# Optimization experiments

Measured on AMD Instinct MI355X. Metric: run time of the kernel, lower is better.

## Reference

```python
import jax, jax.numpy as jnp
import numpy as np

N = 50000        # num nodes
E = 800000       # num edges (before self loops)
F_DIM = 256      # embedding_dim
H = 4            # num_heads
C = 64           # latent_dim
SLOPE = 0.2      # PyG GATConv leaky_relu negative_slope


def setup_inputs() -> dict:
    key = jax.random.key(0)
    ks = jax.random.split(key, 11)
    s = 0.05
    return {
        "x": jax.random.normal(ks[0], (N, F_DIM), jnp.float32),
        "edge_index": jax.random.randint(ks[1], (2, E), 0, N),
        "W1": jax.random.normal(ks[2], (F_DIM, H * C), jnp.float32) * s,
        "a_src1": jax.random.normal(ks[3], (H, C), jnp.float32) * s,
        "a_dst1": jax.random.normal(ks[4], (H, C), jnp.float32) * s,
        "b1": jnp.zeros((H * C,), jnp.float32),
        "W2": jax.random.normal(ks[5], (H * C, F_DIM), jnp.float32) * s,
        "a_src2": jax.random.normal(ks[6], (1, F_DIM), jnp.float32) * s,
        "a_dst2": jax.random.normal(ks[7], (1, F_DIM), jnp.float32) * s,
        "b2": jnp.zeros((F_DIM,), jnp.float32),
    }


def gat_layer(x, src, dst, W, a_src, a_dst, bias, heads, out_ch):
    n = x.shape[0]
    xW = (x @ W).reshape(n, heads, out_ch)              # [N,H,C]
    alpha_s = jnp.sum(xW * a_src, axis=-1)               # [N,H]
    alpha_d = jnp.sum(xW * a_dst, axis=-1)               # [N,H]
    e = jax.nn.leaky_relu(alpha_s[src] + alpha_d[dst], SLOPE)  # [E,H]
    m = jax.ops.segment_max(e, dst, num_segments=n)      # segment-softmax over in-edges
    w = jnp.exp(e - m[dst])
    z = jax.ops.segment_sum(w, dst, num_segments=n)
    alpha = w / z[dst]                                    # [E,H]
    out = jax.ops.segment_sum(xW[src] * alpha[:, :, None], dst, num_segments=n)  # [N,H,C]
    return out.reshape(n, heads * out_ch) + bias          # concat=True


def reference(x, edge_index, W1, a_src1, a_dst1, b1, W2, a_src2, a_dst2, b2):
    loop = jnp.arange(N)  # PyG default add_self_loops=True
    src = jnp.concatenate([edge_index[0], loop])
    dst = jnp.concatenate([edge_index[1], loop])
    h = jax.nn.elu(gat_layer(x, src, dst, W1, a_src1, a_dst1, b1, H, C))
    return gat_layer(h, src, dst, W2, a_src2, a_dst2, b2, 1, F_DIM)
```

## Files before the change

### kernel.cpp

```cpp
#include <hip/hip_runtime.h>
#include <hip/hip_bf16.h>
#include <math.h>

#define N_NODES 50000
#define N_EDGES 800000
#define ETOT    (N_EDGES + N_NODES)
#define FDIM    256
#define SLOPE   0.2f

typedef __bf16    bf16x8 __attribute__((ext_vector_type(8)));
typedef float     f32x4  __attribute__((ext_vector_type(4)));
typedef _Float16  f16x8  __attribute__((ext_vector_type(8)));
typedef _Float16  f16x4  __attribute__((ext_vector_type(4)));

__global__ void count_edges(const int* __restrict__ dst, int* __restrict__ counts) {
    int i = blockIdx.x * blockDim.x + threadIdx.x;
    if (i < N_EDGES) atomicAdd(&counts[dst[i]], 1);
}

__global__ void scan1(const int* __restrict__ counts, int* __restrict__ partial,
                      int* __restrict__ blockSums) {
    __shared__ int wsum[4];
    int b = blockIdx.x, t = threadIdx.x;
    int base = b * 1024;
    int i0 = base + t * 4;
    int v[4];
#pragma unroll
    for (int u = 0; u < 4; u++) { int i = i0 + u; v[u] = (i < N_NODES) ? (counts[i] + 1) : 0; }
    v[1] += v[0]; v[2] += v[1]; v[3] += v[2];
    int lane = t & 63, wid = t >> 6;
    int incl = v[3];
#pragma unroll
    for (int d = 1; d < 64; d <<= 1) {
        int o = __shfl_up(incl, d, 64);
        if (lane >= d) incl += o;
    }
    if (lane == 63) wsum[wid] = incl;
    __syncthreads();
    int woff = 0;
#pragma unroll
    for (int w = 0; w < 4; w++) if (w < wid) woff += wsum[w];
    int texcl = woff + incl - v[3];
#pragma unroll
    for (int u = 0; u < 4; u++) { int i = i0 + u; if (i < N_NODES) partial[i] = texcl + v[u]; }
    if (t == 255) blockSums[b] = woff + incl;
}

__global__ void scan3(const int* __restrict__ partial, const int* __restrict__ blockSums,
                      int* __restrict__ row_ptr, int* __restrict__ cursor) {
    int b = blockIdx.x, t = threadIdx.x;
    __shared__ int s_off;
    if (t < 64) {
        int v = (t < b) ? blockSums[t] : 0;
#pragma unroll
        for (int d = 1; d < 64; d <<= 1) v += __shfl_xor(v, d, 64);
        if (t == 0) s_off = v;
    }
    __syncthreads();
    int off = s_off;
    int base = b * 1024;
#pragma unroll
    for (int u = 0; u < 4; u++) {
        int i = base + t + u * 256;
        if (i < N_NODES) {
            row_ptr[i + 1] = off + partial[i];
            cursor[i]      = off + ((i == base) ? 0 : partial[i - 1]);
        }
    }
    if (b == 0 && t == 0) row_ptr[0] = 0;
}

__global__ void scatter_edges(const int* __restrict__ src, const int* __restrict__ dst,
                              int* __restrict__ cursor, int* __restrict__ col_src) {
    int i = blockIdx.x * blockDim.x + threadIdx.x;
    if (i >= ETOT) return;
    int s, d;
    if (i < N_EDGES) { s = src[i]; d = dst[i]; }
    else             { s = i - N_EDGES; d = s; }
    int p = atomicAdd(&cursor[d], 1);
    col_src[p] = s;
}

__global__ void pack_w2(const float* __restrict__ W1, const float* __restrict__ W2,
                        __bf16* __restrict__ P1, __bf16* __restrict__ P2) {
    int tid = blockIdx.x * 256 + threadIdx.x;
    const float* W = (tid < 65536) ? W1 : W2;
    __bf16* P = (tid < 65536) ? P1 : P2;
    int t = tid & 65535;
    int j    = t & 7;
    int lane = (t >> 3) & 63;
    int nb   = (t >> 9) & 3;
    int w    = (t >> 11) & 3;
    int step = (t >> 13) & 7;
    int col = (w << 6) | (nb << 4) | (lane & 15);
    int k   = (step << 5) | ((lane >> 4) << 3) | j;
    float v = W[(k << 8) | col];
    __bf16 h = (__bf16)v;
    int base = (((((step << 2) | w) << 2) | nb) << 10) | (lane << 3) | j;
    P[base]       = h;
    P[base + 512] = (__bf16)(v - (float)h);
}

template <int HEADS, typename AT>
__global__ __launch_bounds__(256) void gemm_mfma(
        const AT* __restrict__ A, const __bf16* __restrict__ Bpk,
        _Float16* __restrict__ Ch,
        const float* __restrict__ avS, const float* __restrict__ avD,
        float* __restrict__ aS, float* __restrict__ aD, int M) {
    constexpr int LDA = 40;
    constexpr int LDC = 272;
    __shared__ union SMem {
        struct { __bf16 Ah[2][128 * LDA]; __bf16 Al[2][128 * LDA]; } st;
        _Float16 cts[64][LDC];
    } smem;
    __shared__ float sred[2][64][4];

    const int t = threadIdx.x;
    const int w = t >> 6, l = t & 63;
    const int q = l >> 4, c16 = l & 15;
    const int row0 = blockIdx.x * 128;

    const int ar = t >> 1, ak = (t & 1) << 4;
    const bool arow_ok = (row0 + ar) < M;
    const AT* Arow = A + (size_t)(row0 + ar) * 256 + ak;

    f32x4 acc[8][4];
#pragma unroll
    for (int i = 0; i < 8; i++)
#pragma unroll
        for (int j = 0; j < 4; j++) acc[i][j] = (f32x4){0.f, 0.f, 0.f, 0.f};

    float4 pv[4];
    f16x8  pvh[2];
#pragma unroll
    for (int i = 0; i < 4; i++) pv[i] = make_float4(0.f, 0.f, 0.f, 0.f);
    pvh[0] = (f16x8){0,0,0,0,0,0,0,0}; pvh[1] = pvh[0];
    if (arow_ok) {
        if constexpr (sizeof(AT) == 4) {
#pragma unroll
            for (int i = 0; i < 4; i++) pv[i] = *(const float4*)(Arow + (i << 2));
        } else {
            pvh[0] = *(const f16x8*)(Arow);
            pvh[1] = *(const f16x8*)(Arow + 8);
        }
    }

    for (int step = 0; step < 8; ++step) {
        const int k0 = step << 5;
        const int buf = step & 1;

        {
            float vv[16];
            if constexpr (sizeof(AT) == 4) {
#pragma unroll
                for (int i = 0; i < 4; i++) {
                    vv[i * 4 + 0] = pv[i].x; vv[i * 4 + 1] = pv[i].y;
                    vv[i * 4 + 2] = pv[i].z; vv[i * 4 + 3] = pv[i].w;
                }
            } else {
#pragma unroll
                for (int i = 0; i < 16; i++) vv[i] = (float)pvh[i >> 3][i & 7];
            }
            bf16x8 hv[2], lv[2];
#pragma unroll
            for (int i = 0; i < 16; i++) {
                __bf16 hb = (__bf16)vv[i];
                hv[i >> 3][i & 7] = hb;
                lv[i >> 3][i & 7] = (__bf16)(vv[i] - (float)hb);
            }
            *(bf16x8*)(&smem.st.Ah[buf][ar * LDA + ak])     = hv[0];
            *(bf16x8*)(&smem.st.Ah[buf][ar * LDA + ak + 8]) = hv[1];
            *(bf16x8*)(&smem.st.Al[buf][ar * LDA + ak])     = lv[0];
            *(bf16x8*)(&smem.st.Al[buf][ar * LDA + ak + 8]) = lv[1];
        }
        if (step < 7 && arow_ok) {
            if constexpr (sizeof(AT) == 4) {
#pragma unroll
                for (int i = 0; i < 4; i++) pv[i] = *(const float4*)(Arow + k0 + 32 + (i << 2));
            } else {
                pvh[0] = *(const f16x8*)(Arow + k0 + 32);
                pvh[1] = *(const f16x8*)(Arow + k0 + 40);
            }
        }
        const __bf16* Bs = Bpk + ((size_t)((step << 2) | w) << 12);
        bf16x8 bh[4], bl[4];
#pragma unroll
        for (int nb = 0; nb < 4; nb++) {
            bh[nb] = *(const bf16x8*)(Bs + (nb << 10) + (l << 3));
            bl[nb] = *(const bf16x8*)(Bs + (nb << 10) + 512 + (l << 3));
        }
        __syncthreads();

#pragma unroll
        for (int mb = 0; mb < 8; mb++) {
            int off = (c16 + (mb << 4)) * LDA + (q << 3);
            bf16x8 ah  = *(const bf16x8*)(&smem.st.Ah[buf][off]);
            bf16x8 alo = *(const bf16x8*)(&smem.st.Al[buf][off]);
#pragma unroll
            for (int nb = 0; nb < 4; nb++) {
                acc[mb][nb] = __builtin_amdgcn_mfma_f32_16x16x32_bf16(ah,  bh[nb], acc[mb][nb], 0, 0, 0);
                acc[mb][nb] = __builtin_amdgcn_mfma_f32_16x16x32_bf16(ah,  bl[nb], acc[mb][nb], 0, 0, 0);
                acc[mb][nb] = __builtin_amdgcn_mfma_f32_16x16x32_bf16(alo, bh[nb], acc[mb][nb], 0, 0, 0);
            }
        }
    }

#pragma unroll
    for (int half = 0; half < 2; ++half) {
        __syncthreads();
#pragma unroll
        for (int mbl = 0; mbl < 4; mbl++) {
            const int mb = (half << 2) | mbl;
#pragma unroll
            for (int r = 0; r < 4; r++) {
                int row = (mbl << 4) + (q << 2) + r;
                float s = 0.f, d = 0.f;
#pragma unroll
                for (int nb = 0; nb < 4; nb++) {
                    int col = (w << 6) + (nb << 4) + c16;
                    float val = acc[mb][nb][r];
                    s = fmaf(val, avS[col], s);
                    d = fmaf(val, avD[col], d);
                    smem.cts[row][col] = (_Float16)val;
                }
#pragma unroll
                for (int dd = 1; dd < 16; dd <<= 1) {
                    s += __shfl_xor(s, dd, 64);
                    d += __shfl_xor(d, dd, 64);
                }
                if (c16 == 0) { sred[0][row][w] = s; sred[1][row][w] = d; }
            }
        }
        __syncthreads();

        {
            const int crow = t >> 2;
            const int grow = row0 + (half << 6) + crow;
            if (grow < M) {
                _Float16* dstp = Ch + (size_t)grow * 256;
#pragma unroll
                for (int i = 0; i < 8; i++) {
                    int col = ((t & 3) << 3) + (i << 5);
                    *(f16x8*)(dstp + col) = *(const f16x8*)(&smem.cts[crow][col]);
                }
            }
        }
        if (HEADS == 4) {
            int row = t >> 2, wv = t & 3;
            int v = row0 + (half << 6) + row;
            if (v < M) { aS[v * 4 + wv] = sred[0][row][wv]; aD[v * 4 + wv] = sred[1][row][wv]; }
        } else {
            if (t < 64) {
                int v = row0 + (half << 6) + t;
                if (v < M) {
                    aS[v] = sred[0][t][0] + sred[0][t][1] + sred[0][t][2] + sred[0][t][3];
                    aD[v] = sred[1][t][0] + sred[1][t][1] + sred[1][t][2] + sred[1][t][3];
                }
            }
        }
    }
}

template <int HEADS, bool ELU, typename OT>
__global__ __launch_bounds__(256) void gat_aggregate_wave(
        const _Float16* __restrict__ xWh, const float* __restrict__ aS,
        const float* __restrict__ aD, const int* __restrict__ row_ptr,
        const int* __restrict__ col_src, const float* __restrict__ bias,
        OT* __restrict__ out) {
    const int wid  = threadIdx.x >> 6;
    const int lane = threadIdx.x & 63;
    const int v = blockIdx.x * 4 + wid;
    if (v >= N_NODES) return;

    constexpr int CH = 64 / HEADS;
    const int h = (HEADS == 4) ? (lane >> 4) : 0;
    const int q = (HEADS == 4) ? (lane & 15) : lane;

    const int half = lane >> 5;
    const int fl   = lane & 31;
    const int hf   = (HEADS == 4) ? (fl >> 3) : 0;
    const int wbase = (HEADS == 4) ? (hf << 4) : 0;

    const int beg = row_ptr[v], end = row_ptr[v + 1];
    const float adv = aD[v * HEADS + h];

    float acc[8] = {0.f, 0.f, 0.f, 0.f, 0.f, 0.f, 0.f, 0.f};
    float z = 0.f;
    for (int j0 = beg; j0 < end; j0 += CH) {
        const int cnt = min(CH, end - j0);
        int s = 0;
        float wgt = 0.f;
        if (q < cnt) {
            s = col_src[j0 + q];
            float e = aS[s * HEADS + h] + adv;
            e = (e > 0.f) ? e : SLOPE * e;
            wgt = __expf(e);
        }
        z += wgt;
        for (int jj = 0; jj < cnt; jj += 2) {
            const int qm = jj + half;
            const int sl = wbase | qm;
            const int   sj = __shfl(s,   sl, 64);
            const float wj = __shfl(wgt, sl, 64);
            if (qm < cnt) {
                const f16x8 row = *(const f16x8*)(xWh + ((size_t)sj << 8) + (fl << 3));
#pragma unroll
                for (int i = 0; i < 8; i++)
                    acc[i] = fmaf(wj, (float)row[i], acc[i]);
            }
        }
    }
#pragma unroll
    for (int d = 1; d < CH; d <<= 1) z += __shfl_xor(z, d, 64);
    const float zf = (HEADS == 4) ? __shfl(z, hf << 4, 64) : z;

#pragma unroll
    for (int i = 0; i < 8; i++) acc[i] += __shfl_xor(acc[i], 32, 64);

    const float rz = 1.f / zf;
    const int fbase = (fl << 3) + (half << 2);
    const float4 bv = *(const float4*)(bias + fbase);
    float4 o;
    o.x = acc[(half << 2) + 0] * rz + bv.x;
    o.y = acc[(half << 2) + 1] * rz + bv.y;
    o.z = acc[(half << 2) + 2] * rz + bv.z;
    o.w = acc[(half << 2) + 3] * rz + bv.w;
    if (ELU) {
        o.x = (o.x > 0.f) ? o.x : expm1f(o.x);
        o.y = (o.y > 0.f) ? o.y : expm1f(o.y);
        o.z = (o.z > 0.f) ? o.z : expm1f(o.z);
        o.w = (o.w > 0.f) ? o.w : expm1f(o.w);
    }
    if constexpr (sizeof(OT) == 2) {
        f16x4 ov;
        ov[0] = (_Float16)o.x; ov[1] = (_Float16)o.y;
        ov[2] = (_Float16)o.z; ov[3] = (_Float16)o.w;
        *(f16x4*)(out + ((size_t)v << 8) + fbase) = ov;
    } else {
        *(float4*)(out + ((size_t)v << 8) + fbase) = o;
    }
}

extern "C" void kernel_launch(void* const* d_in, const int* in_sizes, int n_in,
                              void* d_out, int out_size, void* d_ws, size_t ws_size,
                              hipStream_t stream) {
    const float* x   = (const float*)d_in[0];
    const int*   ei  = (const int*)d_in[1];
    const float* W1  = (const float*)d_in[2];
    const float* as1 = (const float*)d_in[3];
    const float* ad1 = (const float*)d_in[4];
    const float* b1  = (const float*)d_in[5];
    const float* W2  = (const float*)d_in[6];
    const float* as2 = (const float*)d_in[7];
    const float* ad2 = (const float*)d_in[8];
    const float* b2  = (const float*)d_in[9];
    float* out = (float*)d_out;

    const int* src = ei;
    const int* dst = ei + N_EDGES;

    char* w = (char*)d_ws;
    _Float16* xWh = (_Float16*)w; w += (size_t)N_NODES * 256 * 2;
    _Float16* hh  = (_Float16*)w; w += (size_t)N_NODES * 256 * 2;
    float* aS = (float*)w;  w += (size_t)N_NODES * 4 * 4;
    float* aD = (float*)w;  w += (size_t)N_NODES * 4 * 4;
    int* row_ptr = (int*)w; w += (((size_t)(N_NODES + 1) * 4 + 255) / 256) * 256;
    int* counts  = (int*)w; w += (((size_t)N_NODES * 4 + 255) / 256) * 256;
    int* cursor  = (int*)w; w += (((size_t)N_NODES * 4 + 255) / 256) * 256;
    int* partial = (int*)w; w += (((size_t)N_NODES * 4 + 255) / 256) * 256;
    int* bsums   = (int*)w; w += 256;
    int* col_src = (int*)w; w += (size_t)ETOT * 4;
    __bf16* Wpk1 = (__bf16*)w; w += 131072 * 2;
    __bf16* Wpk2 = (__bf16*)w; w += 131072 * 2;

    int nb = (N_NODES + 1023) / 1024;

    pack_w2<<<512, 256, 0, stream>>>(W1, W2, Wpk1, Wpk2);

    hipMemsetAsync(counts, 0, (size_t)N_NODES * 4, stream);
    count_edges<<<(N_EDGES + 255) / 256, 256, 0, stream>>>(dst, counts);
    scan1<<<nb, 256, 0, stream>>>(counts, partial, bsums);
    scan3<<<nb, 256, 0, stream>>>(partial, bsums, row_ptr, cursor);
    scatter_edges<<<(ETOT + 255) / 256, 256, 0, stream>>>(src, dst, cursor, col_src);

    int gemm_blocks = (N_NODES + 127) / 128;
    int agg_blocks  = (N_NODES + 3) / 4;

    gemm_mfma<4, float><<<gemm_blocks, 256, 0, stream>>>(x, Wpk1, xWh, as1, ad1, aS, aD, N_NODES);
    gat_aggregate_wave<4, true, _Float16><<<agg_blocks, 256, 0, stream>>>(xWh, aS, aD, row_ptr, col_src, b1, hh);

    gemm_mfma<1, _Float16><<<gemm_blocks, 256, 0, stream>>>(hh, Wpk2, xWh, as2, ad2, aS, aD, N_NODES);
    gat_aggregate_wave<1, false, float><<<agg_blocks, 256, 0, stream>>>(xWh, aS, aD, row_ptr, col_src, b2, out);
}
```

Measured before the change: 296.8 us.

## Fuse independent launches into horizontal kernels for count/pack and gemm1/scatter

Merges the edge-count and weight-pack kernels into one launch split by block index. It also merges the first-layer GEMM with the edge-scatter kernel in the same way, so the independent CSR scatter can run alongside the GEMM. This cuts launch count and lets memory-bound atomics overlap compute-bound MFMA work. The trade-off is that the fused GEMM kernel carries the GEMM's shared-memory and register footprint for the scatter blocks too, which may reduce occupancy for the scatter part.

```diff
diff --git a/kernel.cpp b/kernel.cpp
--- a/kernel.cpp
+++ b/kernel.cpp
@@ -8,15 +8,15 @@
 #define FDIM    256
 #define SLOPE   0.2f
 
+#define COUNT_BLOCKS 3125
+#define PACK_BLOCKS  512
+#define GEMM_BLOCKS  ((N_NODES + 127) / 128)
+#define SCAT_BLOCKS  ((ETOT + 255) / 256)
+
 typedef __bf16    bf16x8 __attribute__((ext_vector_type(8)));
 typedef float     f32x4  __attribute__((ext_vector_type(4)));
 typedef _Float16  f16x8  __attribute__((ext_vector_type(8)));
 typedef _Float16  f16x4  __attribute__((ext_vector_type(4)));
-
-__global__ void count_edges(const int* __restrict__ dst, int* __restrict__ counts) {
-    int i = blockIdx.x * blockDim.x + threadIdx.x;
-    if (i < N_EDGES) atomicAdd(&counts[dst[i]], 1);
-}
 
 __global__ void scan1(const int* __restrict__ counts, int* __restrict__ partial,
                       int* __restrict__ blockSums) {
@@ -70,40 +70,37 @@
     if (b == 0 && t == 0) row_ptr[0] = 0;
 }
 
-__global__ void scatter_edges(const int* __restrict__ src, const int* __restrict__ dst,
-                              int* __restrict__ cursor, int* __restrict__ col_src) {
-    int i = blockIdx.x * blockDim.x + threadIdx.x;
-    if (i >= ETOT) return;
-    int s, d;
-    if (i < N_EDGES) { s = src[i]; d = dst[i]; }
-    else             { s = i - N_EDGES; d = s; }
-    int p = atomicAdd(&cursor[d], 1);
-    col_src[p] = s;
-}
-
-__global__ void pack_w2(const float* __restrict__ W1, const float* __restrict__ W2,
-                        __bf16* __restrict__ P1, __bf16* __restrict__ P2) {
-    int tid = blockIdx.x * 256 + threadIdx.x;
-    const float* W = (tid < 65536) ? W1 : W2;
-    __bf16* P = (tid < 65536) ? P1 : P2;
-    int t = tid & 65535;
-    int j    = t & 7;
-    int lane = (t >> 3) & 63;
-    int nb   = (t >> 9) & 3;
-    int w    = (t >> 11) & 3;
-    int step = (t >> 13) & 7;
-    int col = (w << 6) | (nb << 4) | (lane & 15);
-    int k   = (step << 5) | ((lane >> 4) << 3) | j;
-    float v = W[(k << 8) | col];
-    __bf16 h = (__bf16)v;
-    int base = (((((step << 2) | w) << 2) | nb) << 10) | (lane << 3) | j;
-    P[base]       = h;
-    P[base + 512] = (__bf16)(v - (float)h);
+__global__ __launch_bounds__(256) void fat_count_pack(
+        const int* __restrict__ dst, int* __restrict__ counts,
+        const float* __restrict__ W1, const float* __restrict__ W2,
+        __bf16* __restrict__ P1, __bf16* __restrict__ P2) {
+    const int b = blockIdx.x;
+    if (b < COUNT_BLOCKS) {
+        int i = b * 256 + threadIdx.x;
+        if (i < N_EDGES) atomicAdd(&counts[dst[i]], 1);
+    } else {
+        int tid = (b - COUNT_BLOCKS) * 256 + threadIdx.x;
+        const float* W = (tid < 65536) ? W1 : W2;
+        __bf16* P = (tid < 65536) ? P1 : P2;
+        int t = tid & 65535;
+        int j    = t & 7;
+        int lane = (t >> 3) & 63;
+        int nb   = (t >> 9) & 3;
+        int w    = (t >> 11) & 3;
+        int step = (t >> 13) & 7;
+        int col = (w << 6) | (nb << 4) | (lane & 15);
+        int k   = (step << 5) | ((lane >> 4) << 3) | j;
+        float v = W[(k << 8) | col];
+        __bf16 h = (__bf16)v;
+        int base = (((((step << 2) | w) << 2) | nb) << 10) | (lane << 3) | j;
+        P[base]       = h;
+        P[base + 512] = (__bf16)(v - (float)h);
+    }
 }
 
 template <int HEADS, typename AT>
-__global__ __launch_bounds__(256) void gemm_mfma(
-        const AT* __restrict__ A, const __bf16* __restrict__ Bpk,
+__device__ __forceinline__ void gemm_body(
+        int bid, const AT* __restrict__ A, const __bf16* __restrict__ Bpk,
         _Float16* __restrict__ Ch,
         const float* __restrict__ avS, const float* __restrict__ avD,
         float* __restrict__ aS, float* __restrict__ aD, int M) {
@@ -118,7 +115,7 @@
     const int t = threadIdx.x;
     const int w = t >> 6, l = t & 63;
     const int q = l >> 4, c16 = l & 15;
-    const int row0 = blockIdx.x * 128;
+    const int row0 = bid * 128;
 
     const int ar = t >> 1, ak = (t & 1) << 4;
     const bool arow_ok = (row0 + ar) < M;
@@ -257,6 +254,36 @@
                     aD[v] = sred[1][t][0] + sred[1][t][1] + sred[1][t][2] + sred[1][t][3];
                 }
             }
+        }
+    }
+}
+
+template <int HEADS, typename AT>
+__global__ __launch_bounds__(256) void gemm_mfma(
+        const AT* __restrict__ A, const __bf16* __restrict__ Bpk,
+        _Float16* __restrict__ Ch,
+        const float* __restrict__ avS, const float* __restrict__ avD,
+        float* __restrict__ aS, float* __restrict__ aD, int M) {
+    gemm_body<HEADS, AT>(blockIdx.x, A, Bpk, Ch, avS, avD, aS, aD, M);
+}
+
+__global__ __launch_bounds__(256) void fat_gemm1_scatter(
+        const float* __restrict__ A, const __bf16* __restrict__ Bpk,
+        _Float16* __restrict__ Ch,
+        const float* __restrict__ avS, const float* __restrict__ avD,
+        float* __restrict__ aS, float* __restrict__ aD,
+        const int* __restrict__ src, const int* __restrict__ dst,
+        int* __restrict__ cursor, int* __restrict__ col_src) {
+    if (blockIdx.x < GEMM_BLOCKS) {
+        gemm_body<4, float>(blockIdx.x, A, Bpk, Ch, avS, avD, aS, aD, N_NODES);
+    } else {
+        int i = (blockIdx.x - GEMM_BLOCKS) * 256 + threadIdx.x;
+        if (i < ETOT) {
+            int s, d;
+            if (i < N_EDGES) { s = src[i]; d = dst[i]; }
+            else             { s = i - N_EDGES; d = s; }
+            int p = atomicAdd(&cursor[d], 1);
+            col_src[p] = s;
         }
     }
 }
@@ -375,20 +402,17 @@
 
     int nb = (N_NODES + 1023) / 1024;
 
-    pack_w2<<<512, 256, 0, stream>>>(W1, W2, Wpk1, Wpk2);
-
     hipMemsetAsync(counts, 0, (size_t)N_NODES * 4, stream);
-    count_edges<<<(N_EDGES + 255) / 256, 256, 0, stream>>>(dst, counts);
+    fat_count_pack<<<COUNT_BLOCKS + PACK_BLOCKS, 256, 0, stream>>>(dst, counts, W1, W2, Wpk1, Wpk2);
     scan1<<<nb, 256, 0, stream>>>(counts, partial, bsums);
     scan3<<<nb, 256, 0, stream>>>(partial, bsums, row_ptr, cursor);
-    scatter_edges<<<(ETOT + 255) / 256, 256, 0, stream>>>(src, dst, cursor, col_src);
-
-    int gemm_blocks = (N_NODES + 127) / 128;
-    int agg_blocks  = (N_NODES + 3) / 4;
-
-    gemm_mfma<4, float><<<gemm_blocks, 256, 0, stream>>>(x, Wpk1, xWh, as1, ad1, aS, aD, N_NODES);
+
+    int agg_blocks = (N_NODES + 3) / 4;
+
+    fat_gemm1_scatter<<<GEMM_BLOCKS + SCAT_BLOCKS, 256, 0, stream>>>(
+        x, Wpk1, xWh, as1, ad1, aS, aD, src, dst, cursor, col_src);
     gat_aggregate_wave<4, true, _Float16><<<agg_blocks, 256, 0, stream>>>(xWh, aS, aD, row_ptr, col_src, b1, hh);
 
-    gemm_mfma<1, _Float16><<<gemm_blocks, 256, 0, stream>>>(hh, Wpk2, xWh, as2, ad2, aS, aD, N_NODES);
+    gemm_mfma<1, _Float16><<<GEMM_BLOCKS, 256, 0, stream>>>(hh, Wpk2, xWh, as2, ad2, aS, aD, N_NODES);
     gat_aggregate_wave<1, false, float><<<agg_blocks, 256, 0, stream>>>(xWh, aS, aD, row_ptr, col_src, b2, out);
 }
```

Result: faster. 275.7 us (-7.1%).
